# Optimization experiments

Measured on AMD Instinct MI355X. Metric: run time of the kernel, lower is better.

The kernel has to match this reference:

```python
import jax, jax.numpy as jnp
import numpy as np

EPS = 1e-07

def _ciou(preds, targets, eps=EPS):
    # xywh -> corner boxes
    x1, y1, w1, h1 = preds[:, 0], preds[:, 1], preds[:, 2], preds[:, 3]
    x2, y2, w2, h2 = targets[:, 0], targets[:, 1], targets[:, 2], targets[:, 3]
    w1_, h1_, w2_, h2_ = w1 / 2, h1 / 2, w2 / 2, h2 / 2
    b1x1, b1x2, b1y1, b1y2 = x1 - w1_, x1 + w1_, y1 - h1_, y1 + h1_
    b2x1, b2x2, b2y1, b2y2 = x2 - w2_, x2 + w2_, y2 - h2_, y2 + h2_
    # intersection
    iw = jnp.clip(jnp.minimum(b1x2, b2x2) - jnp.maximum(b1x1, b2x1), 0)
    ih = jnp.clip(jnp.minimum(b1y2, b2y2) - jnp.maximum(b1y1, b2y1), 0)
    inter = iw * ih
    union = w1 * h1 + w2 * h2 - inter + eps
    iou = inter / union
    # enclosing box
    cw = jnp.maximum(b1x2, b2x2) - jnp.minimum(b1x1, b2x1)
    ch = jnp.maximum(b1y2, b2y2) - jnp.minimum(b1y1, b2y1)
    c2 = cw * cw + ch * ch + eps  # squared diagonal of enclosing box
    # squared center distance
    rho2 = ((b2x1 + b2x2 - b1x1 - b1x2) ** 2 + (b2y1 + b2y2 - b1y1 - b1y2) ** 2) / 4
    # aspect-ratio consistency term
    v = (4 / np.pi ** 2) * (jnp.arctan(w2 / (h2 + eps)) - jnp.arctan(w1 / (h1 + eps))) ** 2
    alpha = jax.lax.stop_gradient(v / (v - iou + (1 + eps)))  # torch.no_grad in original
    return iou - (rho2 / c2 + v * alpha)


def setup_inputs() -> dict:
    key = jax.random.key(0)
    k1, k2 = jax.random.split(key)
    M = 4_000_000
    preds = jax.random.uniform(k1, (M, 4), dtype=jnp.float32)
    targets = jax.random.uniform(k2, (M, 4), dtype=jnp.float32)
    return {"preds": preds, "targets": targets}


def reference(preds, targets):
    num_targets = targets.shape[0]
    ciou = _ciou(preds, targets)
    # original: sum over per-box (1 - ciou) divided by number of targets
    return jnp.sum(1.0 - ciou) / num_targets
```

## Files before the change

### kernel.cpp

```cpp
#include <hip/hip_runtime.h>
#include <math.h>

#define EPS 1e-7f

__global__ __launch_bounds__(256) void ciou_partial_kernel(
    const float4* __restrict__ preds,
    const float4* __restrict__ targets,
    float* __restrict__ partials,
    int m)
{
    int tid = blockIdx.x * blockDim.x + threadIdx.x;
    int stride = gridDim.x * blockDim.x;

    float acc = 0.0f;
    for (int i = tid; i < m; i += stride) {
        float4 p = preds[i];
        float4 t = targets[i];

        float x1 = p.x, y1 = p.y, w1 = p.z, h1 = p.w;
        float x2 = t.x, y2 = t.y, w2 = t.z, h2 = t.w;

        float w1h = 0.5f * w1, h1h = 0.5f * h1;
        float w2h = 0.5f * w2, h2h = 0.5f * h2;

        float b1x1 = x1 - w1h, b1x2 = x1 + w1h;
        float b1y1 = y1 - h1h, b1y2 = y1 + h1h;
        float b2x1 = x2 - w2h, b2x2 = x2 + w2h;
        float b2y1 = y2 - h2h, b2y2 = y2 + h2h;

        float iw = fmaxf(fminf(b1x2, b2x2) - fmaxf(b1x1, b2x1), 0.0f);
        float ih = fmaxf(fminf(b1y2, b2y2) - fmaxf(b1y1, b2y1), 0.0f);
        float inter = iw * ih;
        float uni = w1 * h1 + w2 * h2 - inter + EPS;
        float iou = inter / uni;

        float cw = fmaxf(b1x2, b2x2) - fminf(b1x1, b2x1);
        float ch = fmaxf(b1y2, b2y2) - fminf(b1y1, b2y1);
        float c2 = cw * cw + ch * ch + EPS;

        float dx = x2 - x1, dy = y2 - y1;
        float rho2 = dx * dx + dy * dy;

        const float c4pi2 = 4.0f / (float)(M_PI * M_PI);
        float da = atanf(w2 / (h2 + EPS)) - atanf(w1 / (h1 + EPS));
        float v = c4pi2 * da * da;
        float alpha = v / (v - iou + (1.0f + EPS));

        float ciou = iou - (rho2 / c2 + v * alpha);
        acc += 1.0f - ciou;
    }

    #pragma unroll
    for (int off = 32; off > 0; off >>= 1)
        acc += __shfl_down(acc, off, 64);

    __shared__ float wsum[4];
    int lane = threadIdx.x & 63;
    int wid  = threadIdx.x >> 6;
    if (lane == 0) wsum[wid] = acc;
    __syncthreads();
    if (threadIdx.x == 0)
        partials[blockIdx.x] = wsum[0] + wsum[1] + wsum[2] + wsum[3];
}

__global__ __launch_bounds__(256) void ciou_final_kernel(
    const float* __restrict__ partials,
    int nblocks,
    float* __restrict__ out,
    float inv_m)
{
    double acc = 0.0;
    for (int i = threadIdx.x; i < nblocks; i += 256)
        acc += (double)partials[i];

    #pragma unroll
    for (int off = 32; off > 0; off >>= 1)
        acc += __shfl_down(acc, off, 64);

    __shared__ double wsum[4];
    int lane = threadIdx.x & 63;
    int wid  = threadIdx.x >> 6;
    if (lane == 0) wsum[wid] = acc;
    __syncthreads();
    if (threadIdx.x == 0)
        out[0] = (float)((wsum[0] + wsum[1] + wsum[2] + wsum[3]) * (double)inv_m);
}

extern "C" void kernel_launch(void* const* d_in, const int* in_sizes, int n_in,
                              void* d_out, int out_size, void* d_ws, size_t ws_size,
                              hipStream_t stream)
{
    const float4* preds   = (const float4*)d_in[0];
    const float4* targets = (const float4*)d_in[1];
    float* out = (float*)d_out;
    float* partials = (float*)d_ws;

    int m = in_sizes[0] / 4;

    int nblocks = 2048;
    size_t max_part = ws_size / sizeof(float);
    if ((size_t)nblocks > max_part) nblocks = (int)max_part;
    if (nblocks < 1) nblocks = 1;

    ciou_partial_kernel<<<nblocks, 256, 0, stream>>>(preds, targets, partials, m);
    ciou_final_kernel<<<1, 256, 0, stream>>>(partials, nblocks, out, 1.0f / (float)m);
}
```

Baseline: 29.86 us.

## Use fast reciprocal, merged atan identity, and 4x unrolled loads in CIoU kernel

Replaces the divisions with hardware approximate reciprocals and folds the two atan calls into one using the atan difference identity, evaluated with a polynomial minimax approximation. The grid-stride loop is unrolled by four, so all loads are issued before any math runs, which raises the number of memory requests in flight. The intent is to cut ALU cost and expose more memory-level parallelism on a 128 MB streaming read, at the cost of slightly lower numerical accuracy.

```diff
diff --git a/kernel.cpp b/kernel.cpp
--- a/kernel.cpp
+++ b/kernel.cpp
@@ -2,6 +2,63 @@
 #include <math.h>
 
 #define EPS 1e-7f
+
+__device__ __forceinline__ float fast_rcp(float x) {
+    return __builtin_amdgcn_rcpf(x);
+}
+
+__device__ __forceinline__ float fast_atan(float q) {
+    float aq  = fabsf(q);
+    float inv = fast_rcp(aq);
+    float t   = fminf(aq, inv);
+    float t2  = t * t;
+    float p = -0.0117212f;
+    p = fmaf(p, t2,  0.05265332f);
+    p = fmaf(p, t2, -0.11643287f);
+    p = fmaf(p, t2,  0.19354346f);
+    p = fmaf(p, t2, -0.33262347f);
+    p = fmaf(p, t2,  0.99997726f);
+    p = p * t;
+    float r = (aq > 1.0f) ? (1.57079632679f - p) : p;
+    return copysignf(r, q);
+}
+
+__device__ __forceinline__ float ciou_loss_elem(float4 p, float4 t) {
+    float x1 = p.x, y1 = p.y, w1 = p.z, h1 = p.w;
+    float x2 = t.x, y2 = t.y, w2 = t.z, h2 = t.w;
+
+    float w1h = 0.5f * w1, h1h = 0.5f * h1;
+    float w2h = 0.5f * w2, h2h = 0.5f * h2;
+
+    float b1x1 = x1 - w1h, b1x2 = x1 + w1h;
+    float b1y1 = y1 - h1h, b1y2 = y1 + h1h;
+    float b2x1 = x2 - w2h, b2x2 = x2 + w2h;
+    float b2y1 = y2 - h2h, b2y2 = y2 + h2h;
+
+    float iw = fmaxf(fminf(b1x2, b2x2) - fmaxf(b1x1, b2x1), 0.0f);
+    float ih = fmaxf(fminf(b1y2, b2y2) - fmaxf(b1y1, b2y1), 0.0f);
+    float inter = iw * ih;
+    float uni = w1 * h1 + w2 * h2 - inter + EPS;
+    float iou = inter * fast_rcp(uni);
+
+    float cw = fmaxf(b1x2, b2x2) - fminf(b1x1, b2x1);
+    float ch = fmaxf(b1y2, b2y2) - fminf(b1y1, b2y1);
+    float c2 = cw * cw + ch * ch + EPS;
+
+    float dx = x2 - x1, dy = y2 - y1;
+    float rho2 = fmaf(dx, dx, dy * dy);
+
+    float h1e = h1 + EPS, h2e = h2 + EPS;
+    float num = w2 * h1e - w1 * h2e;
+    float den = fmaf(h1e, h2e, w1 * w2);
+    float da  = fast_atan(num * fast_rcp(den));
+
+    const float c4pi2 = 4.0f / (float)(M_PI * M_PI);
+    float v = c4pi2 * da * da;
+    float alpha = v * fast_rcp(v - iou + (1.0f + EPS));
+
+    return 1.0f - iou + rho2 * fast_rcp(c2) + v * alpha;
+}
 
 __global__ __launch_bounds__(256) void ciou_partial_kernel(
     const float4* __restrict__ preds,
@@ -9,45 +66,30 @@
     float* __restrict__ partials,
     int m)
 {
+    constexpr int U = 4;
     int tid = blockIdx.x * blockDim.x + threadIdx.x;
-    int stride = gridDim.x * blockDim.x;
+    int S = gridDim.x * blockDim.x;
 
     float acc = 0.0f;
-    for (int i = tid; i < m; i += stride) {
-        float4 p = preds[i];
-        float4 t = targets[i];
-
-        float x1 = p.x, y1 = p.y, w1 = p.z, h1 = p.w;
-        float x2 = t.x, y2 = t.y, w2 = t.z, h2 = t.w;
-
-        float w1h = 0.5f * w1, h1h = 0.5f * h1;
-        float w2h = 0.5f * w2, h2h = 0.5f * h2;
-
-        float b1x1 = x1 - w1h, b1x2 = x1 + w1h;
-        float b1y1 = y1 - h1h, b1y2 = y1 + h1h;
-        float b2x1 = x2 - w2h, b2x2 = x2 + w2h;
-        float b2y1 = y2 - h2h, b2y2 = y2 + h2h;
-
-        float iw = fmaxf(fminf(b1x2, b2x2) - fmaxf(b1x1, b2x1), 0.0f);
-        float ih = fmaxf(fminf(b1y2, b2y2) - fmaxf(b1y1, b2y1), 0.0f);
-        float inter = iw * ih;
-        float uni = w1 * h1 + w2 * h2 - inter + EPS;
-        float iou = inter / uni;
-
-        float cw = fmaxf(b1x2, b2x2) - fminf(b1x1, b2x1);
-        float ch = fmaxf(b1y2, b2y2) - fminf(b1y1, b2y1);
-        float c2 = cw * cw + ch * ch + EPS;
-
-        float dx = x2 - x1, dy = y2 - y1;
-        float rho2 = dx * dx + dy * dy;
-
-        const float c4pi2 = 4.0f / (float)(M_PI * M_PI);
-        float da = atanf(w2 / (h2 + EPS)) - atanf(w1 / (h1 + EPS));
-        float v = c4pi2 * da * da;
-        float alpha = v / (v - iou + (1.0f + EPS));
-
-        float ciou = iou - (rho2 / c2 + v * alpha);
-        acc += 1.0f - ciou;
+    for (int i0 = tid; i0 < m; i0 += S * U) {
+        float4 p[U], t[U];
+        int idx[U];
+        #pragma unroll
+        for (int u = 0; u < U; ++u) {
+            idx[u] = i0 + u * S;
+            if (idx[u] < m) {
+                p[u] = preds[idx[u]];
+                t[u] = targets[idx[u]];
+            } else {
+                p[u] = make_float4(0.f, 0.f, 0.f, 0.f);
+                t[u] = make_float4(0.f, 0.f, 0.f, 0.f);
+            }
+        }
+        #pragma unroll
+        for (int u = 0; u < U; ++u) {
+            float val = ciou_loss_elem(p[u], t[u]);
+            acc += (idx[u] < m) ? val : 0.0f;
+        }
     }
 
     #pragma unroll
```

Result: slower. 31.31 us (+4.9%).
